# Optimization experiments

Hardware: AMD Instinct MI355X
Metric: run time of the kernel (lower is better)

## Reference

```python
import jax, jax.numpy as jnp
import numpy as np

RADIUS = 0.5
HEADS = 4
LATENT = 128
KIN = 3 + 3 + 3 + 1  # q_pos + o_pos + rel + dist
LN_EPS = 1e-5


def setup_inputs() -> dict:
    key = jax.random.key(0)
    ks = jax.random.split(key, 12)
    B, Nq, No = 2, 1024, 1024
    h_obs = jax.random.normal(ks[0], (B, No, LATENT), dtype=jnp.float32)
    pos_obs = jax.random.uniform(ks[1], (B, No, 3), dtype=jnp.float32)
    pos_query = jax.random.uniform(ks[2], (B, Nq, 3), dtype=jnp.float32)
    obs_mask = jax.random.randint(ks[3], (B, No), 0, 2, dtype=jnp.int32)
    # kernel MLP params: Linear(KIN, LATENT) -> ReLU -> Linear(LATENT, HEADS)
    W1 = jax.random.normal(ks[4], (KIN, LATENT), dtype=jnp.float32) * (1.0 / np.sqrt(KIN))
    b1 = jax.random.normal(ks[5], (LATENT,), dtype=jnp.float32) * 0.01
    W2 = jax.random.normal(ks[6], (LATENT, HEADS), dtype=jnp.float32) * (1.0 / np.sqrt(LATENT))
    b2 = jax.random.normal(ks[7], (HEADS,), dtype=jnp.float32) * 0.01
    ln_g = jnp.ones((LATENT,), dtype=jnp.float32)
    ln_b = jnp.zeros((LATENT,), dtype=jnp.float32)
    Wv = jax.random.normal(ks[8], (LATENT, LATENT), dtype=jnp.float32) * (1.0 / np.sqrt(LATENT))
    bv = jax.random.normal(ks[9], (LATENT,), dtype=jnp.float32) * 0.01
    return {"h_obs": h_obs, "pos_obs": pos_obs, "pos_query": pos_query,
            "obs_mask": obs_mask, "W1": W1, "b1": b1, "W2": W2, "b2": b2,
            "ln_g": ln_g, "ln_b": ln_b, "Wv": Wv, "bv": bv}


def reference(h_obs, pos_obs, pos_query, obs_mask, W1, b1, W2, b2, ln_g, ln_b, Wv, bv):
    B, Nq, _ = pos_query.shape
    _, No, _ = pos_obs.shape
    H, D = HEADS, LATENT // HEADS

    # pairwise geometric encoding: (B, Nq, No, *)
    rel = pos_query[:, :, None, :] - pos_obs[:, None, :, :]
    dist = jnp.linalg.norm(rel, axis=-1, keepdims=True)
    q_exp = jnp.broadcast_to(pos_query[:, :, None, :], rel.shape)
    o_exp = jnp.broadcast_to(pos_obs[:, None, :, :], rel.shape)
    kin = jnp.concatenate([q_exp, o_exp, rel, dist], axis=-1)  # (B,Nq,No,KIN)

    # per-pair MLP -> per-head attention logits
    hid = jax.nn.relu(kin @ W1 + b1)                 # (B,Nq,No,LATENT)
    logits = hid @ W2 + b2                           # (B,Nq,No,H)
    logits = jnp.transpose(logits, (0, 3, 1, 2))     # (B,H,Nq,No)

    # radius + observation masking
    neg = jnp.float32(-jnp.inf)
    mask = (dist[..., 0] > RADIUS)[:, None, :, :] | (obs_mask == 0)[:, None, None, :]
    logits = jnp.where(mask, neg, logits)
    weights = jax.nn.softmax(logits, axis=-1)        # (B,H,Nq,No)

    # value path: LayerNorm + projection
    mu = jnp.mean(h_obs, axis=-1, keepdims=True)
    var = jnp.var(h_obs, axis=-1, keepdims=True)
    hn = (h_obs - mu) / jnp.sqrt(var + LN_EPS) * ln_g + ln_b
    v = hn @ Wv + bv                                 # (B,No,LATENT)
    v = jnp.transpose(v.reshape(B, No, H, D), (0, 2, 1, 3))  # (B,H,No,D)

    out = jnp.einsum('bhqo,bhod->bhqd', weights, v)  # (B,H,Nq,D)
    out = jnp.transpose(out, (0, 2, 1, 3)).reshape(B, Nq, H * D)
    return out
```

## Files before the change

### kernel.cpp

```cpp
#include <hip/hip_runtime.h>
#include <math.h>
#include <float.h>

#define B_ 2
#define NQ 1024
#define NO 1024
#define LAT 128
#define NHEADS 4
#define RADIUS_ 0.5f
#define LN_EPS_ 1e-5f
#define TILE 512
#define TILE_P (TILE + 8)

#define V_BYTES ((size_t)B_ * NO * LAT * 4)

__device__ __forceinline__ float selh(int h, float a, float b, float c, float d) {
  return h == 0 ? a : (h == 1 ? b : (h == 2 ? c : d));
}

__global__ __launch_bounds__(256) void gano_prep_kernel(
    const float* __restrict__ h_obs, const float* __restrict__ ln_g,
    const float* __restrict__ ln_b, const float* __restrict__ Wv,
    const float* __restrict__ bv, const float* __restrict__ W1,
    const float* __restrict__ b1, float* __restrict__ v_out,
    float4* __restrict__ Cw, float4* __restrict__ A4, int write_derived)
{
  const int tid = threadIdx.x;
  const int j = tid & 127;
  const int half = tid >> 7;
  const int wave = tid >> 6;
  const int lane = tid & 63;
  const int r0 = blockIdx.x * 4 + half * 2;

  __shared__ float s_redA[2][4];
  __shared__ float s_redB[2][4];
  __shared__ __align__(16) float s_hn[4][LAT];

  const float x0 = h_obs[(size_t)r0 * LAT + j];
  const float x1 = h_obs[(size_t)(r0 + 1) * LAT + j];
  float s0 = x0, s1 = x1;
  #pragma unroll
  for (int off = 32; off >= 1; off >>= 1) {
    s0 += __shfl_down(s0, off);
    s1 += __shfl_down(s1, off);
  }
  if (lane == 0) { s_redA[0][wave] = s0; s_redA[1][wave] = s1; }
  __syncthreads();
  const float mu0 = (s_redA[0][half * 2] + s_redA[0][half * 2 + 1]) * (1.0f / LAT);
  const float mu1 = (s_redA[1][half * 2] + s_redA[1][half * 2 + 1]) * (1.0f / LAT);
  const float d0 = x0 - mu0, d1 = x1 - mu1;
  float q0 = d0 * d0, q1 = d1 * d1;
  #pragma unroll
  for (int off = 32; off >= 1; off >>= 1) {
    q0 += __shfl_down(q0, off);
    q1 += __shfl_down(q1, off);
  }
  if (lane == 0) { s_redB[0][wave] = q0; s_redB[1][wave] = q1; }
  __syncthreads();
  const float var0 = (s_redB[0][half * 2] + s_redB[0][half * 2 + 1]) * (1.0f / LAT);
  const float var1 = (s_redB[1][half * 2] + s_redB[1][half * 2 + 1]) * (1.0f / LAT);
  const float g = ln_g[j], be = ln_b[j];
  s_hn[half * 2 + 0][j] = d0 * rsqrtf(var0 + LN_EPS_) * g + be;
  s_hn[half * 2 + 1][j] = d1 * rsqrtf(var1 + LN_EPS_) * g + be;
  __syncthreads();

  float a0 = 0.0f, a1 = 0.0f;
  const float4* h0 = (const float4*)s_hn[half * 2 + 0];
  const float4* h1 = (const float4*)s_hn[half * 2 + 1];
  #pragma unroll 4
  for (int k4 = 0; k4 < LAT / 4; ++k4) {
    const float4 u0 = h0[k4];
    const float4 u1 = h1[k4];
    const float w0 = Wv[(k4 * 4 + 0) * LAT + j];
    const float w1 = Wv[(k4 * 4 + 1) * LAT + j];
    const float w2 = Wv[(k4 * 4 + 2) * LAT + j];
    const float w3 = Wv[(k4 * 4 + 3) * LAT + j];
    a0 = fmaf(u0.x, w0, a0); a0 = fmaf(u0.y, w1, a0);
    a0 = fmaf(u0.z, w2, a0); a0 = fmaf(u0.w, w3, a0);
    a1 = fmaf(u1.x, w0, a1); a1 = fmaf(u1.y, w1, a1);
    a1 = fmaf(u1.z, w2, a1); a1 = fmaf(u1.w, w3, a1);
  }
  const float bvj = bv[j];
  v_out[(size_t)(r0 + 0) * LAT + j] = a0 + bvj;
  v_out[(size_t)(r0 + 1) * LAT + j] = a1 + bvj;

  if (write_derived && blockIdx.x == 0 && tid < LAT) {
    float w[10];
    #pragma unroll
    for (int k = 0; k < 10; ++k) w[k] = W1[k * LAT + tid];
    Cw[tid] = make_float4(w[3] - w[6], w[4] - w[7], w[5] - w[8], w[9]);
    A4[tid] = make_float4(w[0] + w[6], w[1] + w[7], w[2] + w[8], b1[tid]);
  }
}

template <bool DERIVED>
__device__ __forceinline__ void mlp_logits(
    int t, int Nv, const float* s_Q, const int* s_vidx, const float* s_vdist,
    const float* __restrict__ pob, const float4* __restrict__ Cw,
    const float4* __restrict__ W2v, const float* __restrict__ W1,
    float b20, float b21, float b22, float b23,
    float& l0, float& l1, float& l2, float& l3)
{
  const bool active = t < Nv;
  l0 = l1 = l2 = l3 = -FLT_MAX;
  if (!__any(active)) return;
  const int tt = active ? t : Nv - 1;
  const int idx = s_vidx[tt];
  const float dist = s_vdist[tt];
  const float ox = pob[idx * 3 + 0], oy = pob[idx * 3 + 1], oz = pob[idx * 3 + 2];
  float a0 = b20, a1 = b21, a2 = b22, a3 = b23;
  #pragma unroll 2
  for (int j4 = 0; j4 < LAT / 4; ++j4) {
    const float4 q4 = *(const float4*)&s_Q[j4 << 2];
    #pragma unroll
    for (int u = 0; u < 4; ++u) {
      const int jj = (j4 << 2) + u;
      float4 cw;
      if constexpr (DERIVED) {
        cw = Cw[jj];
      } else {
        cw = make_float4(W1[3 * LAT + jj] - W1[6 * LAT + jj],
                         W1[4 * LAT + jj] - W1[7 * LAT + jj],
                         W1[5 * LAT + jj] - W1[8 * LAT + jj],
                         W1[9 * LAT + jj]);
      }
      const float4 w2 = W2v[jj];
      const float qj = (u == 0) ? q4.x : (u == 1) ? q4.y : (u == 2) ? q4.z : q4.w;
      float gg = fmaf(cw.x, ox, qj);
      gg = fmaf(cw.y, oy, gg);
      gg = fmaf(cw.z, oz, gg);
      gg = fmaf(cw.w, dist, gg);
      gg = fmaxf(gg, 0.0f);
      a0 = fmaf(gg, w2.x, a0);
      a1 = fmaf(gg, w2.y, a1);
      a2 = fmaf(gg, w2.z, a2);
      a3 = fmaf(gg, w2.w, a3);
    }
  }
  if (active) { l0 = a0; l1 = a1; l2 = a2; l3 = a3; }
}

template <bool DERIVED>
__global__ __launch_bounds__(256, 6) void gano_main_kernel(
    const float* __restrict__ pos_obs, const float* __restrict__ pos_query,
    const int* __restrict__ obs_mask,
    const float* __restrict__ W1, const float* __restrict__ b1,
    const float4* __restrict__ W2v, const float* __restrict__ b2,
    const float* __restrict__ v,
    const float4* __restrict__ Cw, const float4* __restrict__ A4,
    float* __restrict__ out)
{
  __shared__ __align__(16) float s_Q[LAT];
  __shared__ int   s_vidx[NO];
  __shared__ float s_vdist[NO];
  __shared__ float s_p[NHEADS][TILE_P];
  __shared__ int   s_cnt[16];
  __shared__ float s_red[NHEADS][4];
  __shared__ float s_zred[NHEADS][4];
  __shared__ __align__(16) float s_part[4][LAT];

  const int tid = threadIdx.x;
  const int wave = tid >> 6, lane = tid & 63;
  const int bid = blockIdx.x;
  const int b = bid >> 10, q = bid & (NQ - 1);

  const float qx = pos_query[((size_t)b * NQ + q) * 3 + 0];
  const float qy = pos_query[((size_t)b * NQ + q) * 3 + 1];
  const float qz = pos_query[((size_t)b * NQ + q) * 3 + 2];

  if (tid < LAT) {
    float a0, a1, a2, a3;
    if constexpr (DERIVED) {
      const float4 a = A4[tid];
      a0 = a.x; a1 = a.y; a2 = a.z; a3 = a.w;
    } else {
      a0 = W1[0 * LAT + tid] + W1[6 * LAT + tid];
      a1 = W1[1 * LAT + tid] + W1[7 * LAT + tid];
      a2 = W1[2 * LAT + tid] + W1[8 * LAT + tid];
      a3 = b1[tid];
    }
    s_Q[tid] = fmaf(qx, a0, fmaf(qy, a1, fmaf(qz, a2, a3)));
  }

  const float* pob = pos_obs + (size_t)b * NO * 3;
  const int*   om  = obs_mask + (size_t)b * NO;
  float dists[4];
  unsigned long long bals[4];
  #pragma unroll
  for (int rd = 0; rd < 4; ++rd) {
    const int o = (rd << 8) + tid;
    const float ox = pob[o * 3 + 0], oy = pob[o * 3 + 1], oz = pob[o * 3 + 2];
    const float rx = qx - ox, ry = qy - oy, rz = qz - oz;
    const float dist = sqrtf(rx * rx + ry * ry + rz * rz);
    const int ok = (om[o] != 0) && (dist <= RADIUS_);
    const unsigned long long bal = __ballot(ok);
    if (lane == 0) s_cnt[(rd << 2) + wave] = __popcll(bal);
    bals[rd] = bal;
    dists[rd] = dist;
  }
  __syncthreads();
  int Nv = 0;
  #pragma unroll
  for (int k = 0; k < 16; ++k) Nv += s_cnt[k];
  #pragma unroll
  for (int rd = 0; rd < 4; ++rd) {
    const int slot = (rd << 2) + wave;
    int base = 0;
    for (int k = 0; k < slot; ++k) base += s_cnt[k];
    if ((bals[rd] >> lane) & 1ull) {
      const int pos = base + __popcll(bals[rd] & ((1ull << lane) - 1ull));
      s_vidx[pos] = (rd << 8) + tid;
      s_vdist[pos] = dists[rd];
    }
  }
  __syncthreads();

  const int c5 = tid & 31;
  const int phase = tid >> 5;
  const int hh = c5 >> 3;
  float ax = 0.f, ay = 0.f, az = 0.f, aw = 0.f;
  float m0 = -FLT_MAX, m1 = -FLT_MAX, m2 = -FLT_MAX, m3 = -FLT_MAX;
  float z0 = 0.f, z1 = 0.f, z2 = 0.f, z3 = 0.f;
  const float b20 = b2[0], b21 = b2[1], b22 = b2[2], b23 = b2[3];
  const float* vb = v + (size_t)b * NO * LAT;
  const float* vcol = vb + (c5 << 2);

  const int ntiles = (Nv + TILE - 1) >> 9;
  for (int tile = 0; tile < ntiles; ++tile) {
    const int tbase = tile << 9;
    float l00, l01, l02, l03, l10, l11, l12, l13;
    mlp_logits<DERIVED>(tbase + tid, Nv, s_Q, s_vidx, s_vdist, pob, Cw, W2v, W1,
                        b20, b21, b22, b23, l00, l01, l02, l03);
    mlp_logits<DERIVED>(tbase + 256 + tid, Nv, s_Q, s_vidx, s_vdist, pob, Cw, W2v, W1,
                        b20, b21, b22, b23, l10, l11, l12, l13);

    float t0 = fmaxf(l00, l10), t1 = fmaxf(l01, l11);
    float t2 = fmaxf(l02, l12), t3 = fmaxf(l03, l13);
    #pragma unroll
    for (int off = 32; off >= 1; off >>= 1) {
      t0 = fmaxf(t0, __shfl_down(t0, off));
      t1 = fmaxf(t1, __shfl_down(t1, off));
      t2 = fmaxf(t2, __shfl_down(t2, off));
      t3 = fmaxf(t3, __shfl_down(t3, off));
    }
    if (lane == 0) { s_red[0][wave] = t0; s_red[1][wave] = t1;
                     s_red[2][wave] = t2; s_red[3][wave] = t3; }
    __syncthreads();
    const float x0 = fmaxf(fmaxf(s_red[0][0], s_red[0][1]), fmaxf(s_red[0][2], s_red[0][3]));
    const float x1 = fmaxf(fmaxf(s_red[1][0], s_red[1][1]), fmaxf(s_red[1][2], s_red[1][3]));
    const float x2 = fmaxf(fmaxf(s_red[2][0], s_red[2][1]), fmaxf(s_red[2][2], s_red[2][3]));
    const float x3 = fmaxf(fmaxf(s_red[3][0], s_red[3][1]), fmaxf(s_red[3][2], s_red[3][3]));
    const float nm0 = fmaxf(m0, x0), nm1 = fmaxf(m1, x1);
    const float nm2 = fmaxf(m2, x2), nm3 = fmaxf(m3, x3);
    const float sc0 = __expf(m0 - nm0), sc1 = __expf(m1 - nm1);
    const float sc2 = __expf(m2 - nm2), sc3 = __expf(m3 - nm3);
    m0 = nm0; m1 = nm1; m2 = nm2; m3 = nm3;

    const float p00 = __expf(l00 - nm0), p01 = __expf(l01 - nm1);
    const float p02 = __expf(l02 - nm2), p03 = __expf(l03 - nm3);
    const float p10 = __expf(l10 - nm0), p11 = __expf(l11 - nm1);
    const float p12 = __expf(l12 - nm2), p13 = __expf(l13 - nm3);
    s_p[0][tid] = p00; s_p[0][256 + tid] = p10;
    s_p[1][tid] = p01; s_p[1][256 + tid] = p11;
    s_p[2][tid] = p02; s_p[2][256 + tid] = p12;
    s_p[3][tid] = p03; s_p[3][256 + tid] = p13;
    float u0 = p00 + p10, u1 = p01 + p11, u2 = p02 + p12, u3 = p03 + p13;
    #pragma unroll
    for (int off = 32; off >= 1; off >>= 1) {
      u0 += __shfl_down(u0, off);
      u1 += __shfl_down(u1, off);
      u2 += __shfl_down(u2, off);
      u3 += __shfl_down(u3, off);
    }
    if (lane == 0) { s_zred[0][wave] = u0; s_zred[1][wave] = u1;
                     s_zred[2][wave] = u2; s_zred[3][wave] = u3; }
    __syncthreads();
    z0 = z0 * sc0 + (s_zred[0][0] + s_zred[0][1] + s_zred[0][2] + s_zred[0][3]);
    z1 = z1 * sc1 + (s_zred[1][0] + s_zred[1][1] + s_zred[1][2] + s_zred[1][3]);
    z2 = z2 * sc2 + (s_zred[2][0] + s_zred[2][1] + s_zred[2][2] + s_zred[2][3]);
    z3 = z3 * sc3 + (s_zred[3][0] + s_zred[3][1] + s_zred[3][2] + s_zred[3][3]);
    const float scme = selh(hh, sc0, sc1, sc2, sc3);
    ax *= scme; ay *= scme; az *= scme; aw *= scme;

    const int tcnt = min(TILE, Nv - tbase);
    int it = phase;
    float bx = 0.f, by = 0.f, bz = 0.f, bw = 0.f;
    for (; it + 8 < tcnt; it += 16) {
      const float pA = s_p[hh][it];
      const float pB = s_p[hh][it + 8];
      const int iA = s_vidx[tbase + it];
      const int iB = s_vidx[tbase + it + 8];
      const float4 vA = *(const float4*)(vcol + (size_t)iA * LAT);
      const float4 vB = *(const float4*)(vcol + (size_t)iB * LAT);
      ax = fmaf(pA, vA.x, ax); ay = fmaf(pA, vA.y, ay);
      az = fmaf(pA, vA.z, az); aw = fmaf(pA, vA.w, aw);
      bx = fmaf(pB, vB.x, bx); by = fmaf(pB, vB.y, by);
      bz = fmaf(pB, vB.z, bz); bw = fmaf(pB, vB.w, bw);
    }
    if (it < tcnt) {
      const float pA = s_p[hh][it];
      const int iA = s_vidx[tbase + it];
      const float4 vA = *(const float4*)(vcol + (size_t)iA * LAT);
      ax = fmaf(pA, vA.x, ax); ay = fmaf(pA, vA.y, ay);
      az = fmaf(pA, vA.z, az); aw = fmaf(pA, vA.w, aw);
    }
    ax += bx; ay += by; az += bz; aw += bw;
    if (tile + 1 < ntiles) __syncthreads();
  }

  ax += __shfl_down(ax, 32);
  ay += __shfl_down(ay, 32);
  az += __shfl_down(az, 32);
  aw += __shfl_down(aw, 32);
  if (lane < 32) {
    *(float4*)&s_part[wave][lane << 2] = make_float4(ax, ay, az, aw);
  }
  __syncthreads();
  if (tid < LAT) {
    const float r4 = s_part[0][tid] + s_part[1][tid] + s_part[2][tid] + s_part[3][tid];
    const int h = tid >> 5;
    const float zz = selh(h, z0, z1, z2, z3);
    const float r = (Nv > 0) ? (r4 / zz) : 0.0f;
    out[((size_t)b * NQ + q) * LAT + tid] = r;
  }
}

extern "C" void kernel_launch(void* const* d_in, const int* in_sizes, int n_in,
                              void* d_out, int out_size, void* d_ws, size_t ws_size,
                              hipStream_t stream) {
  const float* h_obs     = (const float*)d_in[0];
  const float* pos_obs   = (const float*)d_in[1];
  const float* pos_query = (const float*)d_in[2];
  const int*   obs_mask  = (const int*)d_in[3];
  const float* W1        = (const float*)d_in[4];
  const float* b1        = (const float*)d_in[5];
  const float* W2        = (const float*)d_in[6];
  const float* b2        = (const float*)d_in[7];
  const float* ln_g      = (const float*)d_in[8];
  const float* ln_b      = (const float*)d_in[9];
  const float* Wv        = (const float*)d_in[10];
  const float* bv        = (const float*)d_in[11];
  float* outp = (float*)d_out;
  float* v    = (float*)d_ws;

  const size_t need = V_BYTES + 2 * LAT * sizeof(float4);
  const int derived = (ws_size >= need) ? 1 : 0;
  float4* Cw = (float4*)((char*)d_ws + V_BYTES);
  float4* A4 = Cw + LAT;
  if (!derived) { Cw = (float4*)d_ws; A4 = (float4*)d_ws; }

  gano_prep_kernel<<<(B_ * NO) / 4, 256, 0, stream>>>(h_obs, ln_g, ln_b, Wv, bv,
                                                      W1, b1, v, Cw, A4, derived);
  if (derived) {
    gano_main_kernel<true><<<B_ * NQ, 256, 0, stream>>>(
        pos_obs, pos_query, obs_mask, W1, b1, (const float4*)W2, b2, v,
        (const float4*)Cw, (const float4*)A4, outp);
  } else {
    gano_main_kernel<false><<<B_ * NQ, 256, 0, stream>>>(
        pos_obs, pos_query, obs_mask, W1, b1, (const float4*)W2, b2, v,
        (const float4*)Cw, (const float4*)A4, outp);
  }
}
```

Baseline: 39.36 us.

## Pack per-pair MLP into float2 vectors and interleave W1/W2 weights

Each thread now computes logits for two adjacent valid pairs at once using 2-wide float vectors, so the compiler can emit packed FMA/max instructions (v_pk_fma_f32 on CDNA). The derived Cw and W2 rows are interleaved into one CW8 buffer, so one contiguous 32-byte load serves both per hidden unit. The slot assignment is rotated per block by wave, which changes which pairs each wave handles and gives contiguous 2-element LDS stores. This aims to halve the VALU instruction count of the dominant MLP loop. The cost is a different inactive-lane pattern and slightly more workspace.

New measurement: 42.82 us. 1.09x slower.

```diff
diff --git a/kernel.cpp b/kernel.cpp
--- a/kernel.cpp
+++ b/kernel.cpp
@@ -14,16 +14,21 @@
 
 #define V_BYTES ((size_t)B_ * NO * LAT * 4)
 
+typedef float v2f __attribute__((ext_vector_type(2)));
+__device__ __forceinline__ v2f splat2(float x) { return (v2f){x, x}; }
+
 __device__ __forceinline__ float selh(int h, float a, float b, float c, float d) {
   return h == 0 ? a : (h == 1 ? b : (h == 2 ? c : d));
 }
+
 
 __global__ __launch_bounds__(256) void gano_prep_kernel(
     const float* __restrict__ h_obs, const float* __restrict__ ln_g,
     const float* __restrict__ ln_b, const float* __restrict__ Wv,
     const float* __restrict__ bv, const float* __restrict__ W1,
-    const float* __restrict__ b1, float* __restrict__ v_out,
-    float4* __restrict__ Cw, float4* __restrict__ A4, int write_derived)
+    const float* __restrict__ b1, const float* __restrict__ W2,
+    float* __restrict__ v_out,
+    float4* __restrict__ A4, float4* __restrict__ CW8, int write_derived)
 {
   const int tid = threadIdx.x;
   const int j = tid & 127;
@@ -88,56 +93,11 @@
     float w[10];
     #pragma unroll
     for (int k = 0; k < 10; ++k) w[k] = W1[k * LAT + tid];
-    Cw[tid] = make_float4(w[3] - w[6], w[4] - w[7], w[5] - w[8], w[9]);
     A4[tid] = make_float4(w[0] + w[6], w[1] + w[7], w[2] + w[8], b1[tid]);
-  }
-}
-
-template <bool DERIVED>
-__device__ __forceinline__ void mlp_logits(
-    int t, int Nv, const float* s_Q, const int* s_vidx, const float* s_vdist,
-    const float* __restrict__ pob, const float4* __restrict__ Cw,
-    const float4* __restrict__ W2v, const float* __restrict__ W1,
-    float b20, float b21, float b22, float b23,
-    float& l0, float& l1, float& l2, float& l3)
-{
-  const bool active = t < Nv;
-  l0 = l1 = l2 = l3 = -FLT_MAX;
-  if (!__any(active)) return;
-  const int tt = active ? t : Nv - 1;
-  const int idx = s_vidx[tt];
-  const float dist = s_vdist[tt];
-  const float ox = pob[idx * 3 + 0], oy = pob[idx * 3 + 1], oz = pob[idx * 3 + 2];
-  float a0 = b20, a1 = b21, a2 = b22, a3 = b23;
-  #pragma unroll 2
-  for (int j4 = 0; j4 < LAT / 4; ++j4) {
-    const float4 q4 = *(const float4*)&s_Q[j4 << 2];
-    #pragma unroll
-    for (int u = 0; u < 4; ++u) {
-      const int jj = (j4 << 2) + u;
-      float4 cw;
-      if constexpr (DERIVED) {
-        cw = Cw[jj];
-      } else {
-        cw = make_float4(W1[3 * LAT + jj] - W1[6 * LAT + jj],
-                         W1[4 * LAT + jj] - W1[7 * LAT + jj],
-                         W1[5 * LAT + jj] - W1[8 * LAT + jj],
-                         W1[9 * LAT + jj]);
-      }
-      const float4 w2 = W2v[jj];
-      const float qj = (u == 0) ? q4.x : (u == 1) ? q4.y : (u == 2) ? q4.z : q4.w;
-      float gg = fmaf(cw.x, ox, qj);
-      gg = fmaf(cw.y, oy, gg);
-      gg = fmaf(cw.z, oz, gg);
-      gg = fmaf(cw.w, dist, gg);
-      gg = fmaxf(gg, 0.0f);
-      a0 = fmaf(gg, w2.x, a0);
-      a1 = fmaf(gg, w2.y, a1);
-      a2 = fmaf(gg, w2.z, a2);
-      a3 = fmaf(gg, w2.w, a3);
-    }
-  }
-  if (active) { l0 = a0; l1 = a1; l2 = a2; l3 = a3; }
+    CW8[2 * tid + 0] = make_float4(w[3] - w[6], w[4] - w[7], w[5] - w[8], w[9]);
+    CW8[2 * tid + 1] = make_float4(W2[tid * NHEADS + 0], W2[tid * NHEADS + 1],
+                                   W2[tid * NHEADS + 2], W2[tid * NHEADS + 3]);
+  }
 }
 
 template <bool DERIVED>
@@ -147,7 +107,7 @@
     const float* __restrict__ W1, const float* __restrict__ b1,
     const float4* __restrict__ W2v, const float* __restrict__ b2,
     const float* __restrict__ v,
-    const float4* __restrict__ Cw, const float4* __restrict__ A4,
+    const float4* __restrict__ A4, const float4* __restrict__ CW8,
     float* __restrict__ out)
 {
   __shared__ __align__(16) float s_Q[LAT];
@@ -218,24 +178,64 @@
   const int c5 = tid & 31;
   const int phase = tid >> 5;
   const int hh = c5 >> 3;
+  const int vslot = (((wave + bid) & 3) << 7) + (lane << 1);
+
   float ax = 0.f, ay = 0.f, az = 0.f, aw = 0.f;
   float m0 = -FLT_MAX, m1 = -FLT_MAX, m2 = -FLT_MAX, m3 = -FLT_MAX;
   float z0 = 0.f, z1 = 0.f, z2 = 0.f, z3 = 0.f;
   const float b20 = b2[0], b21 = b2[1], b22 = b2[2], b23 = b2[3];
-  const float* vb = v + (size_t)b * NO * LAT;
-  const float* vcol = vb + (c5 << 2);
+  const float* vcol = v + (size_t)b * NO * LAT + (c5 << 2);
 
   const int ntiles = (Nv + TILE - 1) >> 9;
   for (int tile = 0; tile < ntiles; ++tile) {
     const int tbase = tile << 9;
-    float l00, l01, l02, l03, l10, l11, l12, l13;
-    mlp_logits<DERIVED>(tbase + tid, Nv, s_Q, s_vidx, s_vdist, pob, Cw, W2v, W1,
-                        b20, b21, b22, b23, l00, l01, l02, l03);
-    mlp_logits<DERIVED>(tbase + 256 + tid, Nv, s_Q, s_vidx, s_vdist, pob, Cw, W2v, W1,
-                        b20, b21, b22, b23, l10, l11, l12, l13);
-
-    float t0 = fmaxf(l00, l10), t1 = fmaxf(l01, l11);
-    float t2 = fmaxf(l02, l12), t3 = fmaxf(l03, l13);
+    const int tA = tbase + vslot, tB = tA + 1;
+    const bool aA = tA < Nv, aB = tB < Nv;
+    v2f L0 = splat2(-FLT_MAX), L1 = L0, L2 = L0, L3 = L0;
+    if (__any(aA)) {
+      const int cA = aA ? tA : Nv - 1;
+      const int cB = aB ? tB : Nv - 1;
+      const int iA = s_vidx[cA], iB = s_vidx[cB];
+      const v2f dd = {s_vdist[cA], s_vdist[cB]};
+      const v2f ox2 = {pob[iA * 3 + 0], pob[iB * 3 + 0]};
+      const v2f oy2 = {pob[iA * 3 + 1], pob[iB * 3 + 1]};
+      const v2f oz2 = {pob[iA * 3 + 2], pob[iB * 3 + 2]};
+      v2f A0 = splat2(b20), A1 = splat2(b21), A2 = splat2(b22), A3 = splat2(b23);
+      #pragma unroll 2
+      for (int j4 = 0; j4 < LAT / 4; ++j4) {
+        const float4 q4 = *(const float4*)&s_Q[j4 << 2];
+        #pragma unroll
+        for (int u = 0; u < 4; ++u) {
+          const int jj = (j4 << 2) + u;
+          float4 cw, w2;
+          if constexpr (DERIVED) {
+            cw = CW8[2 * jj + 0];
+            w2 = CW8[2 * jj + 1];
+          } else {
+            cw = make_float4(W1[3 * LAT + jj] - W1[6 * LAT + jj],
+                             W1[4 * LAT + jj] - W1[7 * LAT + jj],
+                             W1[5 * LAT + jj] - W1[8 * LAT + jj],
+                             W1[9 * LAT + jj]);
+            w2 = W2v[jj];
+          }
+          const float qj = (u == 0) ? q4.x : (u == 1) ? q4.y : (u == 2) ? q4.z : q4.w;
+          v2f gg = __builtin_elementwise_fma(ox2, splat2(cw.x), splat2(qj));
+          gg = __builtin_elementwise_fma(oy2, splat2(cw.y), gg);
+          gg = __builtin_elementwise_fma(oz2, splat2(cw.z), gg);
+          gg = __builtin_elementwise_fma(dd,  splat2(cw.w), gg);
+          gg = __builtin_elementwise_max(gg, splat2(0.0f));
+          A0 = __builtin_elementwise_fma(gg, splat2(w2.x), A0);
+          A1 = __builtin_elementwise_fma(gg, splat2(w2.y), A1);
+          A2 = __builtin_elementwise_fma(gg, splat2(w2.z), A2);
+          A3 = __builtin_elementwise_fma(gg, splat2(w2.w), A3);
+        }
+      }
+      if (aA) { L0.x = A0.x; L1.x = A1.x; L2.x = A2.x; L3.x = A3.x; }
+      if (aB) { L0.y = A0.y; L1.y = A1.y; L2.y = A2.y; L3.y = A3.y; }
+    }
+
+    float t0 = fmaxf(L0.x, L0.y), t1 = fmaxf(L1.x, L1.y);
+    float t2 = fmaxf(L2.x, L2.y), t3 = fmaxf(L3.x, L3.y);
     #pragma unroll
     for (int off = 32; off >= 1; off >>= 1) {
       t0 = fmaxf(t0, __shfl_down(t0, off));
@@ -256,15 +256,15 @@
     const float sc2 = __expf(m2 - nm2), sc3 = __expf(m3 - nm3);
     m0 = nm0; m1 = nm1; m2 = nm2; m3 = nm3;
 
-    const float p00 = __expf(l00 - nm0), p01 = __expf(l01 - nm1);
-    const float p02 = __expf(l02 - nm2), p03 = __expf(l03 - nm3);
-    const float p10 = __expf(l10 - nm0), p11 = __expf(l11 - nm1);
-    const float p12 = __expf(l12 - nm2), p13 = __expf(l13 - nm3);
-    s_p[0][tid] = p00; s_p[0][256 + tid] = p10;
-    s_p[1][tid] = p01; s_p[1][256 + tid] = p11;
-    s_p[2][tid] = p02; s_p[2][256 + tid] = p12;
-    s_p[3][tid] = p03; s_p[3][256 + tid] = p13;
-    float u0 = p00 + p10, u1 = p01 + p11, u2 = p02 + p12, u3 = p03 + p13;
+    const v2f P0 = {__expf(L0.x - nm0), __expf(L0.y - nm0)};
+    const v2f P1 = {__expf(L1.x - nm1), __expf(L1.y - nm1)};
+    const v2f P2 = {__expf(L2.x - nm2), __expf(L2.y - nm2)};
+    const v2f P3 = {__expf(L3.x - nm3), __expf(L3.y - nm3)};
+    *(v2f*)&s_p[0][vslot] = P0;
+    *(v2f*)&s_p[1][vslot] = P1;
+    *(v2f*)&s_p[2][vslot] = P2;
+    *(v2f*)&s_p[3][vslot] = P3;
+    float u0 = P0.x + P0.y, u1 = P1.x + P1.y, u2 = P2.x + P2.y, u3 = P3.x + P3.y;
     #pragma unroll
     for (int off = 32; off >= 1; off >>= 1) {
       u0 += __shfl_down(u0, off);
@@ -343,21 +343,21 @@
   float* outp = (float*)d_out;
   float* v    = (float*)d_ws;
 
-  const size_t need = V_BYTES + 2 * LAT * sizeof(float4);
+  const size_t need = V_BYTES + 3 * LAT * sizeof(float4);
   const int derived = (ws_size >= need) ? 1 : 0;
-  float4* Cw = (float4*)((char*)d_ws + V_BYTES);
-  float4* A4 = Cw + LAT;
-  if (!derived) { Cw = (float4*)d_ws; A4 = (float4*)d_ws; }
+  float4* A4  = (float4*)((char*)d_ws + V_BYTES);
+  float4* CW8 = A4 + LAT;
+  if (!derived) { A4 = (float4*)d_ws; CW8 = (float4*)d_ws; }
 
   gano_prep_kernel<<<(B_ * NO) / 4, 256, 0, stream>>>(h_obs, ln_g, ln_b, Wv, bv,
-                                                      W1, b1, v, Cw, A4, derived);
+                                                      W1, b1, W2, v, A4, CW8, derived);
   if (derived) {
     gano_main_kernel<true><<<B_ * NQ, 256, 0, stream>>>(
         pos_obs, pos_query, obs_mask, W1, b1, (const float4*)W2, b2, v,
-        (const float4*)Cw, (const float4*)A4, outp);
+        (const float4*)A4, (const float4*)CW8, outp);
   } else {
     gano_main_kernel<false><<<B_ * NQ, 256, 0, stream>>>(
         pos_obs, pos_query, obs_mask, W1, b1, (const float4*)W2, b2, v,
-        (const float4*)Cw, (const float4*)A4, outp);
+        (const float4*)A4, (const float4*)CW8, outp);
   }
 }
```

## Use per-wave online softmax and merge wave partials at the end

Applied to the files above, without the earlier changes.

Restructures the main kernel so each wave independently processes 64-candidate chunks with its own running max and sum, and the four waves' partial results are merged once at the end. This removes the block-wide barriers and shared reductions that the old code ran per 512-candidate tile. The MLP weights (derived W1 terms and W2) now live in shared memory per block rather than coming from global memory or a precomputed buffer. Occupancy hint rises to 8 blocks per CU. In exchange, each wave now gathers V rows as float2 per lane instead of float4, and the final merge needs extra exp evaluations.

Measured after the change: 45.96 us. 16.8% more time.

```diff
diff --git a/kernel.cpp b/kernel.cpp
--- a/kernel.cpp
+++ b/kernel.cpp
@@ -9,8 +9,7 @@
 #define NHEADS 4
 #define RADIUS_ 0.5f
 #define LN_EPS_ 1e-5f
-#define TILE 512
-#define TILE_P (TILE + 8)
+#define PW_STRIDE 68
 
 #define V_BYTES ((size_t)B_ * NO * LAT * 4)
 
@@ -21,9 +20,7 @@
 __global__ __launch_bounds__(256) void gano_prep_kernel(
     const float* __restrict__ h_obs, const float* __restrict__ ln_g,
     const float* __restrict__ ln_b, const float* __restrict__ Wv,
-    const float* __restrict__ bv, const float* __restrict__ W1,
-    const float* __restrict__ b1, float* __restrict__ v_out,
-    float4* __restrict__ Cw, float4* __restrict__ A4, int write_derived)
+    const float* __restrict__ bv, float* __restrict__ v_out)
 {
   const int tid = threadIdx.x;
   const int j = tid & 127;
@@ -83,81 +80,22 @@
   const float bvj = bv[j];
   v_out[(size_t)(r0 + 0) * LAT + j] = a0 + bvj;
   v_out[(size_t)(r0 + 1) * LAT + j] = a1 + bvj;
-
-  if (write_derived && blockIdx.x == 0 && tid < LAT) {
-    float w[10];
-    #pragma unroll
-    for (int k = 0; k < 10; ++k) w[k] = W1[k * LAT + tid];
-    Cw[tid] = make_float4(w[3] - w[6], w[4] - w[7], w[5] - w[8], w[9]);
-    A4[tid] = make_float4(w[0] + w[6], w[1] + w[7], w[2] + w[8], b1[tid]);
-  }
 }
 
-template <bool DERIVED>
-__device__ __forceinline__ void mlp_logits(
-    int t, int Nv, const float* s_Q, const int* s_vidx, const float* s_vdist,
-    const float* __restrict__ pob, const float4* __restrict__ Cw,
-    const float4* __restrict__ W2v, const float* __restrict__ W1,
-    float b20, float b21, float b22, float b23,
-    float& l0, float& l1, float& l2, float& l3)
-{
-  const bool active = t < Nv;
-  l0 = l1 = l2 = l3 = -FLT_MAX;
-  if (!__any(active)) return;
-  const int tt = active ? t : Nv - 1;
-  const int idx = s_vidx[tt];
-  const float dist = s_vdist[tt];
-  const float ox = pob[idx * 3 + 0], oy = pob[idx * 3 + 1], oz = pob[idx * 3 + 2];
-  float a0 = b20, a1 = b21, a2 = b22, a3 = b23;
-  #pragma unroll 2
-  for (int j4 = 0; j4 < LAT / 4; ++j4) {
-    const float4 q4 = *(const float4*)&s_Q[j4 << 2];
-    #pragma unroll
-    for (int u = 0; u < 4; ++u) {
-      const int jj = (j4 << 2) + u;
-      float4 cw;
-      if constexpr (DERIVED) {
-        cw = Cw[jj];
-      } else {
-        cw = make_float4(W1[3 * LAT + jj] - W1[6 * LAT + jj],
-                         W1[4 * LAT + jj] - W1[7 * LAT + jj],
-                         W1[5 * LAT + jj] - W1[8 * LAT + jj],
-                         W1[9 * LAT + jj]);
-      }
-      const float4 w2 = W2v[jj];
-      const float qj = (u == 0) ? q4.x : (u == 1) ? q4.y : (u == 2) ? q4.z : q4.w;
-      float gg = fmaf(cw.x, ox, qj);
-      gg = fmaf(cw.y, oy, gg);
-      gg = fmaf(cw.z, oz, gg);
-      gg = fmaf(cw.w, dist, gg);
-      gg = fmaxf(gg, 0.0f);
-      a0 = fmaf(gg, w2.x, a0);
-      a1 = fmaf(gg, w2.y, a1);
-      a2 = fmaf(gg, w2.z, a2);
-      a3 = fmaf(gg, w2.w, a3);
-    }
-  }
-  if (active) { l0 = a0; l1 = a1; l2 = a2; l3 = a3; }
-}
-
-template <bool DERIVED>
-__global__ __launch_bounds__(256, 6) void gano_main_kernel(
+__global__ __launch_bounds__(256, 8) void gano_main_kernel(
     const float* __restrict__ pos_obs, const float* __restrict__ pos_query,
     const int* __restrict__ obs_mask,
     const float* __restrict__ W1, const float* __restrict__ b1,
-    const float4* __restrict__ W2v, const float* __restrict__ b2,
-    const float* __restrict__ v,
-    const float4* __restrict__ Cw, const float4* __restrict__ A4,
-    float* __restrict__ out)
+    const float* __restrict__ W2, const float* __restrict__ b2,
+    const float* __restrict__ v, float* __restrict__ out)
 {
-  __shared__ __align__(16) float s_Q[LAT];
   __shared__ int   s_vidx[NO];
   __shared__ float s_vdist[NO];
-  __shared__ float s_p[NHEADS][TILE_P];
+  __shared__ __align__(16) float s_w[LAT][8];
+  __shared__ __align__(16) float s_Q[LAT];
+  __shared__ __align__(16) float s_pw[4][NHEADS][PW_STRIDE];
+  __shared__ float s_mz[4][2][NHEADS];
   __shared__ int   s_cnt[16];
-  __shared__ float s_red[NHEADS][4];
-  __shared__ float s_zred[NHEADS][4];
-  __shared__ __align__(16) float s_part[4][LAT];
 
   const int tid = threadIdx.x;
   const int wave = tid >> 6, lane = tid & 63;
@@ -169,17 +107,17 @@
   const float qz = pos_query[((size_t)b * NQ + q) * 3 + 2];
 
   if (tid < LAT) {
-    float a0, a1, a2, a3;
-    if constexpr (DERIVED) {
-      const float4 a = A4[tid];
-      a0 = a.x; a1 = a.y; a2 = a.z; a3 = a.w;
-    } else {
-      a0 = W1[0 * LAT + tid] + W1[6 * LAT + tid];
-      a1 = W1[1 * LAT + tid] + W1[7 * LAT + tid];
-      a2 = W1[2 * LAT + tid] + W1[8 * LAT + tid];
-      a3 = b1[tid];
-    }
-    s_Q[tid] = fmaf(qx, a0, fmaf(qy, a1, fmaf(qz, a2, a3)));
+    const int j = tid;
+    float w[10];
+    #pragma unroll
+    for (int k = 0; k < 10; ++k) w[k] = W1[k * LAT + j];
+    s_w[j][0] = w[3] - w[6];
+    s_w[j][1] = w[4] - w[7];
+    s_w[j][2] = w[5] - w[8];
+    s_w[j][3] = w[9];
+    const float4 w2r = *(const float4*)&W2[j * NHEADS];
+    s_w[j][4] = w2r.x; s_w[j][5] = w2r.y; s_w[j][6] = w2r.z; s_w[j][7] = w2r.w;
+    s_Q[j] = b1[j] + qx * (w[0] + w[6]) + qy * (w[1] + w[7]) + qz * (w[2] + w[8]);
   }
 
   const float* pob = pos_obs + (size_t)b * NO * 3;
@@ -215,112 +153,125 @@
   }
   __syncthreads();
 
-  const int c5 = tid & 31;
-  const int phase = tid >> 5;
-  const int hh = c5 >> 3;
-  float ax = 0.f, ay = 0.f, az = 0.f, aw = 0.f;
+  const int c0 = lane << 1;
+  const int hh = lane >> 4;
+  const float* vbl = v + (size_t)b * NO * LAT + c0;
+  const float b20 = b2[0], b21 = b2[1], b22 = b2[2], b23 = b2[3];
+
   float m0 = -FLT_MAX, m1 = -FLT_MAX, m2 = -FLT_MAX, m3 = -FLT_MAX;
   float z0 = 0.f, z1 = 0.f, z2 = 0.f, z3 = 0.f;
-  const float b20 = b2[0], b21 = b2[1], b22 = b2[2], b23 = b2[3];
-  const float* vb = v + (size_t)b * NO * LAT;
-  const float* vcol = vb + (c5 << 2);
-
-  const int ntiles = (Nv + TILE - 1) >> 9;
-  for (int tile = 0; tile < ntiles; ++tile) {
-    const int tbase = tile << 9;
-    float l00, l01, l02, l03, l10, l11, l12, l13;
-    mlp_logits<DERIVED>(tbase + tid, Nv, s_Q, s_vidx, s_vdist, pob, Cw, W2v, W1,
-                        b20, b21, b22, b23, l00, l01, l02, l03);
-    mlp_logits<DERIVED>(tbase + 256 + tid, Nv, s_Q, s_vidx, s_vdist, pob, Cw, W2v, W1,
-                        b20, b21, b22, b23, l10, l11, l12, l13);
-
-    float t0 = fmaxf(l00, l10), t1 = fmaxf(l01, l11);
-    float t2 = fmaxf(l02, l12), t3 = fmaxf(l03, l13);
+  float ax = 0.f, ay = 0.f;
+
+  for (int cbase = wave << 6; cbase < Nv; cbase += 256) {
+    const int cnt = min(64, Nv - cbase);
+    const bool act = lane < cnt;
+    const int slot = cbase + (act ? lane : (cnt - 1));
+    const int idx = s_vidx[slot];
+    const float dist = s_vdist[slot];
+    const float ox = pob[idx * 3 + 0], oy = pob[idx * 3 + 1], oz = pob[idx * 3 + 2];
+
+    float a0 = b20, a1 = b21, a2 = b22, a3 = b23;
+    #pragma unroll 2
+    for (int j4 = 0; j4 < LAT / 4; ++j4) {
+      const float4 q4 = *(const float4*)&s_Q[j4 << 2];
+      #pragma unroll
+      for (int u = 0; u < 4; ++u) {
+        const int j = (j4 << 2) + u;
+        const float4 cw = *(const float4*)&s_w[j][0];
+        const float4 w2 = *(const float4*)&s_w[j][4];
+        const float qj = (u == 0) ? q4.x : (u == 1) ? q4.y : (u == 2) ? q4.z : q4.w;
+        float gg = fmaf(cw.x, ox, qj);
+        gg = fmaf(cw.y, oy, gg);
+        gg = fmaf(cw.z, oz, gg);
+        gg = fmaf(cw.w, dist, gg);
+        gg = fmaxf(gg, 0.0f);
+        a0 = fmaf(gg, w2.x, a0);
+        a1 = fmaf(gg, w2.y, a1);
+        a2 = fmaf(gg, w2.z, a2);
+        a3 = fmaf(gg, w2.w, a3);
+      }
+    }
+    const float l0 = act ? a0 : -FLT_MAX;
+    const float l1 = act ? a1 : -FLT_MAX;
+    const float l2 = act ? a2 : -FLT_MAX;
+    const float l3 = act ? a3 : -FLT_MAX;
+
+    float x0 = l0, x1 = l1, x2 = l2, x3 = l3;
     #pragma unroll
-    for (int off = 32; off >= 1; off >>= 1) {
-      t0 = fmaxf(t0, __shfl_down(t0, off));
-      t1 = fmaxf(t1, __shfl_down(t1, off));
-      t2 = fmaxf(t2, __shfl_down(t2, off));
-      t3 = fmaxf(t3, __shfl_down(t3, off));
-    }
-    if (lane == 0) { s_red[0][wave] = t0; s_red[1][wave] = t1;
-                     s_red[2][wave] = t2; s_red[3][wave] = t3; }
-    __syncthreads();
-    const float x0 = fmaxf(fmaxf(s_red[0][0], s_red[0][1]), fmaxf(s_red[0][2], s_red[0][3]));
-    const float x1 = fmaxf(fmaxf(s_red[1][0], s_red[1][1]), fmaxf(s_red[1][2], s_red[1][3]));
-    const float x2 = fmaxf(fmaxf(s_red[2][0], s_red[2][1]), fmaxf(s_red[2][2], s_red[2][3]));
-    const float x3 = fmaxf(fmaxf(s_red[3][0], s_red[3][1]), fmaxf(s_red[3][2], s_red[3][3]));
+    for (int off = 1; off < 64; off <<= 1) {
+      x0 = fmaxf(x0, __shfl_xor(x0, off));
+      x1 = fmaxf(x1, __shfl_xor(x1, off));
+      x2 = fmaxf(x2, __shfl_xor(x2, off));
+      x3 = fmaxf(x3, __shfl_xor(x3, off));
+    }
     const float nm0 = fmaxf(m0, x0), nm1 = fmaxf(m1, x1);
     const float nm2 = fmaxf(m2, x2), nm3 = fmaxf(m3, x3);
     const float sc0 = __expf(m0 - nm0), sc1 = __expf(m1 - nm1);
     const float sc2 = __expf(m2 - nm2), sc3 = __expf(m3 - nm3);
     m0 = nm0; m1 = nm1; m2 = nm2; m3 = nm3;
 
-    const float p00 = __expf(l00 - nm0), p01 = __expf(l01 - nm1);
-    const float p02 = __expf(l02 - nm2), p03 = __expf(l03 - nm3);
-    const float p10 = __expf(l10 - nm0), p11 = __expf(l11 - nm1);
-    const float p12 = __expf(l12 - nm2), p13 = __expf(l13 - nm3);
-    s_p[0][tid] = p00; s_p[0][256 + tid] = p10;
-    s_p[1][tid] = p01; s_p[1][256 + tid] = p11;
-    s_p[2][tid] = p02; s_p[2][256 + tid] = p12;
-    s_p[3][tid] = p03; s_p[3][256 + tid] = p13;
-    float u0 = p00 + p10, u1 = p01 + p11, u2 = p02 + p12, u3 = p03 + p13;
+    const float p0 = __expf(l0 - nm0);
+    const float p1 = __expf(l1 - nm1);
+    const float p2 = __expf(l2 - nm2);
+    const float p3 = __expf(l3 - nm3);
+    s_pw[wave][0][lane] = p0;
+    s_pw[wave][1][lane] = p1;
+    s_pw[wave][2][lane] = p2;
+    s_pw[wave][3][lane] = p3;
+    z0 = z0 * sc0 + p0;
+    z1 = z1 * sc1 + p1;
+    z2 = z2 * sc2 + p2;
+    z3 = z3 * sc3 + p3;
+    const float sch = selh(hh, sc0, sc1, sc2, sc3);
+    ax *= sch; ay *= sch;
+
+    const float* pr = s_pw[wave][hh];
+    for (int it = 0; it < cnt; it += 4) {
+      const float4 pq = *(const float4*)&pr[it];
+      const int4 iq = *(const int4*)&s_vidx[cbase + it];
+      const int i0 = iq.x & (NO - 1), i1 = iq.y & (NO - 1);
+      const int i2 = iq.z & (NO - 1), i3 = iq.w & (NO - 1);
+      const float2 v0 = *(const float2*)(vbl + (size_t)i0 * LAT);
+      const float2 v1 = *(const float2*)(vbl + (size_t)i1 * LAT);
+      const float2 v2 = *(const float2*)(vbl + (size_t)i2 * LAT);
+      const float2 v3 = *(const float2*)(vbl + (size_t)i3 * LAT);
+      ax = fmaf(pq.x, v0.x, ax); ay = fmaf(pq.x, v0.y, ay);
+      ax = fmaf(pq.y, v1.x, ax); ay = fmaf(pq.y, v1.y, ay);
+      ax = fmaf(pq.z, v2.x, ax); ay = fmaf(pq.z, v2.y, ay);
+      ax = fmaf(pq.w, v3.x, ax); ay = fmaf(pq.w, v3.y, ay);
+    }
+  }
+
+  #pragma unroll
+  for (int off = 1; off < 64; off <<= 1) {
+    z0 += __shfl_xor(z0, off);
+    z1 += __shfl_xor(z1, off);
+    z2 += __shfl_xor(z2, off);
+    z3 += __shfl_xor(z3, off);
+  }
+  if (lane == 0) {
+    s_mz[wave][0][0] = m0; s_mz[wave][0][1] = m1;
+    s_mz[wave][0][2] = m2; s_mz[wave][0][3] = m3;
+    s_mz[wave][1][0] = z0; s_mz[wave][1][1] = z1;
+    s_mz[wave][1][2] = z2; s_mz[wave][1][3] = z3;
+  }
+  float* part = &s_pw[wave][0][0];
+  part[c0] = ax; part[c0 + 1] = ay;
+  __syncthreads();
+
+  if (tid < LAT) {
+    const int h = tid >> 5;
+    const float mw0 = s_mz[0][0][h], mw1 = s_mz[1][0][h];
+    const float mw2 = s_mz[2][0][h], mw3 = s_mz[3][0][h];
+    const float M = fmaxf(fmaxf(mw0, mw1), fmaxf(mw2, mw3));
+    float num = 0.f, den = 0.f;
     #pragma unroll
-    for (int off = 32; off >= 1; off >>= 1) {
-      u0 += __shfl_down(u0, off);
-      u1 += __shfl_down(u1, off);
-      u2 += __shfl_down(u2, off);
-      u3 += __shfl_down(u3, off);
-    }
-    if (lane == 0) { s_zred[0][wave] = u0; s_zred[1][wave] = u1;
-                     s_zred[2][wave] = u2; s_zred[3][wave] = u3; }
-    __syncthreads();
-    z0 = z0 * sc0 + (s_zred[0][0] + s_zred[0][1] + s_zred[0][2] + s_zred[0][3]);
-    z1 = z1 * sc1 + (s_zred[1][0] + s_zred[1][1] + s_zred[1][2] + s_zred[1][3]);
-    z2 = z2 * sc2 + (s_zred[2][0] + s_zred[2][1] + s_zred[2][2] + s_zred[2][3]);
-    z3 = z3 * sc3 + (s_zred[3][0] + s_zred[3][1] + s_zred[3][2] + s_zred[3][3]);
-    const float scme = selh(hh, sc0, sc1, sc2, sc3);
-    ax *= scme; ay *= scme; az *= scme; aw *= scme;
-
-    const int tcnt = min(TILE, Nv - tbase);
-    int it = phase;
-    float bx = 0.f, by = 0.f, bz = 0.f, bw = 0.f;
-    for (; it + 8 < tcnt; it += 16) {
-      const float pA = s_p[hh][it];
-      const float pB = s_p[hh][it + 8];
-      const int iA = s_vidx[tbase + it];
-      const int iB = s_vidx[tbase + it + 8];
-      const float4 vA = *(const float4*)(vcol + (size_t)iA * LAT);
-      const float4 vB = *(const float4*)(vcol + (size_t)iB * LAT);
-      ax = fmaf(pA, vA.x, ax); ay = fmaf(pA, vA.y, ay);
-      az = fmaf(pA, vA.z, az); aw = fmaf(pA, vA.w, aw);
-      bx = fmaf(pB, vB.x, bx); by = fmaf(pB, vB.y, by);
-      bz = fmaf(pB, vB.z, bz); bw = fmaf(pB, vB.w, bw);
-    }
-    if (it < tcnt) {
-      const float pA = s_p[hh][it];
-      const int iA = s_vidx[tbase + it];
-      const float4 vA = *(const float4*)(vcol + (size_t)iA * LAT);
-      ax = fmaf(pA, vA.x, ax); ay = fmaf(pA, vA.y, ay);
-      az = fmaf(pA, vA.z, az); aw = fmaf(pA, vA.w, aw);
-    }
-    ax += bx; ay += by; az += bz; aw += bw;
-    if (tile + 1 < ntiles) __syncthreads();
-  }
-
-  ax += __shfl_down(ax, 32);
-  ay += __shfl_down(ay, 32);
-  az += __shfl_down(az, 32);
-  aw += __shfl_down(aw, 32);
-  if (lane < 32) {
-    *(float4*)&s_part[wave][lane << 2] = make_float4(ax, ay, az, aw);
-  }
-  __syncthreads();
-  if (tid < LAT) {
-    const float r4 = s_part[0][tid] + s_part[1][tid] + s_part[2][tid] + s_part[3][tid];
-    const int h = tid >> 5;
-    const float zz = selh(h, z0, z1, z2, z3);
-    const float r = (Nv > 0) ? (r4 / zz) : 0.0f;
+    for (int w = 0; w < 4; ++w) {
+      const float e = __expf(s_mz[w][0][h] - M);
+      num = fmaf(e, (&s_pw[w][0][0])[tid], num);
+      den = fmaf(e, s_mz[w][1][h], den);
+    }
+    const float r = (Nv > 0) ? (num / den) : 0.0f;
     out[((size_t)b * NQ + q) * LAT + tid] = r;
   }
 }
@@ -343,21 +294,7 @@
   float* outp = (float*)d_out;
   float* v    = (float*)d_ws;
 
-  const size_t need = V_BYTES + 2 * LAT * sizeof(float4);
-  const int derived = (ws_size >= need) ? 1 : 0;
-  float4* Cw = (float4*)((char*)d_ws + V_BYTES);
-  float4* A4 = Cw + LAT;
-  if (!derived) { Cw = (float4*)d_ws; A4 = (float4*)d_ws; }
-
-  gano_prep_kernel<<<(B_ * NO) / 4, 256, 0, stream>>>(h_obs, ln_g, ln_b, Wv, bv,
-                                                      W1, b1, v, Cw, A4, derived);
-  if (derived) {
-    gano_main_kernel<true><<<B_ * NQ, 256, 0, stream>>>(
-        pos_obs, pos_query, obs_mask, W1, b1, (const float4*)W2, b2, v,
-        (const float4*)Cw, (const float4*)A4, outp);
-  } else {
-    gano_main_kernel<false><<<B_ * NQ, 256, 0, stream>>>(
-        pos_obs, pos_query, obs_mask, W1, b1, (const float4*)W2, b2, v,
-        (const float4*)Cw, (const float4*)A4, outp);
-  }
+  gano_prep_kernel<<<(B_ * NO) / 4, 256, 0, stream>>>(h_obs, ln_g, ln_b, Wv, bv, v);
+  gano_main_kernel<<<B_ * NQ, 256, 0, stream>>>(pos_obs, pos_query, obs_mask,
+                                                W1, b1, W2, b2, v, outp);
 }
```
